# Kernel tuning notes

Hardware: AMD Instinct MI355X
Metric: run time of the kernel (lower is better)

The kernel has to match this reference:

```python
import jax, jax.numpy as jnp
import numpy as np

N = 50000          # nodes
E = 800000         # edges (avg degree 16)
NODE_IN, NODE_OUT = 64, 96
EDGE_IN, EDGE_OUT = 32, 32
CONV = [192, 192]  # hidden_conv_sizes
LIN = [192]        # hidden_linear_sizes
NUM_CLASSES = 2


def _linear_init(k, fan_in, fan_out):
    s = 1.0 / np.sqrt(fan_in)
    kw, kb = jax.random.split(k)
    W = jax.random.uniform(kw, (fan_in, fan_out), jnp.float32, -s, s)
    b = jax.random.uniform(kb, (fan_out,), jnp.float32, -s, s)
    return W, b


def setup_inputs() -> dict:
    key = jax.random.key(0)
    ks = jax.random.split(key, 10)
    node_feats = jax.random.normal(ks[0], (N, NODE_IN), jnp.float32)
    edge_feats = jax.random.normal(ks[1], (E, EDGE_IN), jnp.float32)
    src = jax.random.randint(ks[2], (E,), 0, N)
    dst = jax.random.randint(ks[3], (E,), 0, N)
    Wn, bn = _linear_init(ks[4], NODE_IN, NODE_OUT)
    We, be = _linear_init(ks[5], EDGE_IN, EDGE_OUT)
    Wc0, bc0 = _linear_init(ks[6], NODE_OUT + EDGE_OUT, CONV[0])
    Wc1, bc1 = _linear_init(ks[7], CONV[0], CONV[1])
    Wl0, bl0 = _linear_init(ks[8], CONV[1], LIN[0])
    Wo, bo = _linear_init(ks[9], LIN[0], NUM_CLASSES)
    return dict(node_feats=node_feats, edge_feats=edge_feats,
                Wn=Wn, bn=bn, We=We, be=be,
                Wc0=Wc0, bc0=bc0, Wc1=Wc1, bc1=bc1,
                Wl0=Wl0, bl0=bl0, Wo=Wo, bo=bo,
                src=src, dst=dst)


def reference(node_feats, edge_feats, Wn, bn, We, be, Wc0, bc0, Wc1, bc1,
              Wl0, bl0, Wo, bo, src, dst):
    ones = jnp.ones((E,), jnp.float32)
    deg_in = jnp.clip(jax.ops.segment_sum(ones, dst, num_segments=N), 1.0)
    deg_out = jnp.clip(jax.ops.segment_sum(ones, src, num_segments=N), 1.0)
    inv_in = jax.lax.rsqrt(deg_in)    # D_in^{-1/2}
    inv_out = jax.lax.rsqrt(deg_out)  # D_out^{-1/2}

    # EdgeLayer: per-edge linear, mean-aggregated onto destination nodes
    eh = edge_feats @ We + be                                   # [E, EDGE_OUT]
    edge_h = jax.nn.relu(
        jax.ops.segment_sum(eh, dst, num_segments=N) / deg_in[:, None])

    # NodeEmbeddingLayer: per-node linear
    node_h = jax.nn.relu(node_feats @ Wn + bn)                  # [N, NODE_OUT]

    h = jnp.concatenate([edge_h, node_h], axis=1)               # [N, EDGE_OUT+NODE_OUT]

    # dgl GraphConv (norm='both'): D_in^{-1/2} A D_out^{-1/2} h W + b
    # dropout is identity in eval mode
    for W, b in ((Wc0, bc0), (Wc1, bc1)):
        msg = (h * inv_out[:, None])[src]                       # [E, d] gather
        agg = jax.ops.segment_sum(msg, dst, num_segments=N) * inv_in[:, None]
        h = jax.nn.relu(agg @ W + b)

    h = jax.nn.relu(h @ Wl0 + bl0)
    return h @ Wo + bo                                          # [N, NUM_CLASSES]
```

## Files before the change

kernel.cpp:

```cpp
#include <hip/hip_runtime.h>

#define NN 50000
#define NE 800000
#define CAP 64

typedef unsigned short u16;
typedef __attribute__((ext_vector_type(8))) short bf8_t;
typedef __attribute__((ext_vector_type(4))) float f4_t;

__device__ __forceinline__ u16 f2b(float f) {
    unsigned u = __float_as_uint(f);
    unsigned r = u + 0x7FFF + ((u >> 16) & 1);
    return (u16)(r >> 16);
}

__global__ void build_k(const int* __restrict__ src, const int* __restrict__ dst,
                        int* __restrict__ cursor_in, int* __restrict__ deg_out,
                        int2* __restrict__ csr, int E) {
    int e = blockIdx.x * 256 + threadIdx.x;
    if (e < E) {
        int s = src[e];
        int d = dst[e];
        int p = atomicAdd(cursor_in + d, 1);
        csr[(d << 6) + p] = make_int2(s, e);
        atomicAdd(deg_out + s, 1);
    }
}

__global__ void make_inv_k(const int* __restrict__ deg_in, const int* __restrict__ deg_out,
                           float* __restrict__ inv_in, float* __restrict__ inv_out,
                           float* __restrict__ inv_mean, float* __restrict__ bcoef, int n) {
    int i = blockIdx.x * 256 + threadIdx.x;
    if (i < n) {
        int d_in = deg_in[i];
        float di = fmaxf((float)d_in, 1.0f);
        float dq = fmaxf((float)deg_out[i], 1.0f);
        inv_in[i]   = 1.0f / sqrtf(di);
        inv_out[i]  = 1.0f / sqrtf(dq);
        inv_mean[i] = 1.0f / di;
        bcoef[i]    = (d_in > 0) ? 1.0f : 0.0f;
    }
}

__global__ __launch_bounds__(256) void gather_e2_k(
    const float* __restrict__ ef, const int2* __restrict__ csr,
    const int* __restrict__ deg, float* __restrict__ efa) {
    const int lane = threadIdx.x & 63;
    const int node = __builtin_amdgcn_readfirstlane(blockIdx.x * 4 + (threadIdx.x >> 6));
    const int beg = node << 6;
    const int cnt = deg[node];
    const int off = lane & 31;
    const int half = lane >> 5;
    float acc = 0.0f;

    const int np = cnt >> 1;
    const int nb = np >> 3, rem = np & 7;
    int idx[8];
    if (nb > 0) {
#pragma unroll
        for (int j = 0; j < 8; ++j) idx[j] = csr[beg + 2 * j + half].y;
    }
    for (int b = 0; b < nb; ++b) {
        float lv[8];
#pragma unroll
        for (int j = 0; j < 8; ++j) lv[j] = ef[(size_t)idx[j] * 32 + off];
        int nidx[8];
        const int nbase = beg + 2 * (b + 1) * 8;
        if (b + 1 < nb) {
#pragma unroll
            for (int j = 0; j < 8; ++j) nidx[j] = csr[nbase + 2 * j + half].y;
        }
#pragma unroll
        for (int j = 0; j < 8; ++j) acc += lv[j];
        if (b + 1 < nb) {
#pragma unroll
            for (int j = 0; j < 8; ++j) idx[j] = nidx[j];
        }
    }
    const int tbase = beg + 2 * nb * 8;
    for (int t = 0; t < rem; ++t) acc += ef[(size_t)csr[tbase + 2 * t + half].y * 32 + off];
    if ((cnt & 1) && half == 0) acc += ef[(size_t)csr[beg + cnt - 1].y * 32 + off];

    acc += __shfl_down(acc, 32);
    if (lane < 32) efa[(size_t)node * 32 + off] = acc;
}

template <int D, int LPT>
__global__ __launch_bounds__(256) void gather_b2_k(
    const u16* __restrict__ h, const int2* __restrict__ csr,
    const int* __restrict__ deg, const float* __restrict__ inv_in,
    u16* __restrict__ agg) {
    constexpr int ACT = D / LPT;
    constexpr int NW = LPT / 2;
    const int lane = threadIdx.x & 63;
    const int node = __builtin_amdgcn_readfirstlane(blockIdx.x * 4 + (threadIdx.x >> 6));
    const int beg = node << 6;
    const int cnt = deg[node];
    const int off = (lane < ACT ? lane : ACT - 1) * LPT;

    float acc[LPT];
#pragma unroll
    for (int j = 0; j < LPT; ++j) acc[j] = 0.0f;

    const int nb = cnt >> 3, rem = cnt & 7;
    int idx[8];
    if (nb > 0) {
#pragma unroll
        for (int j = 0; j < 8; ++j) idx[j] = csr[beg + j].x;
    }
    for (int b = 0; b < nb; ++b) {
        unsigned lv[8][NW];
#pragma unroll
        for (int j = 0; j < 8; ++j) {
            const unsigned* p = (const unsigned*)(h + (size_t)idx[j] * D + off);
            if constexpr (NW == 2) {
                uint2 t = *(const uint2*)p;
                lv[j][0] = t.x; lv[j][1] = t.y;
            } else {
                lv[j][0] = *p;
            }
        }
        int nidx[8];
        const int nbase = beg + (b + 1) * 8;
        if (b + 1 < nb) {
#pragma unroll
            for (int j = 0; j < 8; ++j) nidx[j] = csr[nbase + j].x;
        }
#pragma unroll
        for (int j = 0; j < 8; ++j)
#pragma unroll
            for (int q = 0; q < NW; ++q) {
                unsigned u = lv[j][q];
                acc[2 * q]     += __uint_as_float(u << 16);
                acc[2 * q + 1] += __uint_as_float(u & 0xffff0000u);
            }
        if (b + 1 < nb) {
#pragma unroll
            for (int j = 0; j < 8; ++j) idx[j] = nidx[j];
        }
    }
    const int tbase = beg + nb * 8;
    for (int t = 0; t < rem; ++t) {
        const unsigned* p = (const unsigned*)(h + (size_t)csr[tbase + t].x * D + off);
#pragma unroll
        for (int q = 0; q < NW; ++q) {
            unsigned u = p[q];
            acc[2 * q]     += __uint_as_float(u << 16);
            acc[2 * q + 1] += __uint_as_float(u & 0xffff0000u);
        }
    }

    if (lane < ACT) {
        float sc = inv_in[node];
        unsigned o[NW];
#pragma unroll
        for (int q = 0; q < NW; ++q)
            o[q] = (unsigned)f2b(acc[2 * q] * sc) | ((unsigned)f2b(acc[2 * q + 1] * sc) << 16);
        unsigned* dp = (unsigned*)(agg + (size_t)node * D + off);
        if constexpr (NW == 2) {
            uint2 t; t.x = o[0]; t.y = o[1];
            *(uint2*)dp = t;
        } else {
            *dp = o[0];
        }
    }
}

template <int D_IN, int D_OUT, bool SCALE, bool BROW>
__global__ __launch_bounds__(256) void gemm_tile_k(
    const float* __restrict__ in, int in_stride,
    const float* __restrict__ W, const float* __restrict__ bias,
    const float* __restrict__ scale, const float* __restrict__ brow,
    const float* __restrict__ posts,
    u16* __restrict__ out, int out_stride, int n) {
    constexpr int TMW = 8;
    constexpr int ROWS = TMW * 4;
    constexpr int NOUT = (D_OUT + 63) / 64;
    __shared__ float s_in[ROWS * D_IN];

    const int tid = threadIdx.x;
    const int lane = tid & 63;
    const int wave = tid >> 6;
    const int row0 = blockIdx.x * ROWS;

    constexpr int NV = ROWS * D_IN / 4;
    for (int i = tid; i < NV; i += 256) {
        int m = i / (D_IN / 4);
        int kv = i % (D_IN / 4);
        int row = min(row0 + m, n - 1);
        float4 v = *(const float4*)(in + (size_t)row * in_stride + kv * 4);
        if (SCALE) {
            float s = scale[row];
            v.x *= s; v.y *= s; v.z *= s; v.w *= s;
        }
        *(float4*)(s_in + m * D_IN + kv * 4) = v;
    }
    __syncthreads();

    int f[NOUT], ff[NOUT];
    bool fok[NOUT];
    float bv[NOUT];
#pragma unroll
    for (int o = 0; o < NOUT; ++o) {
        f[o] = lane + 64 * o;
        fok[o] = (f[o] < D_OUT);
        ff[o] = fok[o] ? f[o] : 0;
        bv[o] = bias[ff[o]];
    }

    const float* s_my = s_in + wave * TMW * D_IN;

    float acc[NOUT][TMW];
#pragma unroll
    for (int o = 0; o < NOUT; ++o)
#pragma unroll
        for (int m = 0; m < TMW; ++m) acc[o][m] = 0.0f;

    for (int k = 0; k < D_IN; k += 4) {
        float w[4][NOUT];
#pragma unroll
        for (int j = 0; j < 4; ++j)
#pragma unroll
            for (int o = 0; o < NOUT; ++o) w[j][o] = W[(k + j) * D_OUT + ff[o]];
#pragma unroll
        for (int m = 0; m < TMW; ++m) {
            float4 a = *(const float4*)(s_my + m * D_IN + k);
#pragma unroll
            for (int o = 0; o < NOUT; ++o) {
                acc[o][m] = fmaf(a.x, w[0][o], acc[o][m]);
                acc[o][m] = fmaf(a.y, w[1][o], acc[o][m]);
                acc[o][m] = fmaf(a.z, w[2][o], acc[o][m]);
                acc[o][m] = fmaf(a.w, w[3][o], acc[o][m]);
            }
        }
    }

#pragma unroll
    for (int m = 0; m < TMW; ++m) {
        int row = row0 + wave * TMW + m;
        if (row < n) {
            float bc = BROW ? brow[row] : 1.0f;
            float pm = posts[row];
#pragma unroll
            for (int o = 0; o < NOUT; ++o) {
                if (!fok[o]) continue;
                float v = fmaxf(acc[o][m] + bv[o] * bc, 0.0f) * pm;
                out[(size_t)row * out_stride + f[o]] = f2b(v);
            }
        }
    }
}

template <int K>
__global__ void pack_w_k(const float* __restrict__ W, u16* __restrict__ Wp) {
    constexpr int KS = K / 32;
    int idx = blockIdx.x * 256 + threadIdx.x;
    if (idx >= 12 * KS * 64) return;
    int l = idx & 63;
    int s = (idx >> 6) % KS;
    int t = (idx >> 6) / KS;
    int col = t * 16 + (l & 15);
    int krow = s * 32 + ((l >> 4) * 8);
    u16 tmp[8] __attribute__((aligned(16)));
#pragma unroll
    for (int j = 0; j < 8; ++j) tmp[j] = f2b(W[(size_t)(krow + j) * 192 + col]);
    *(uint4*)(Wp + (size_t)idx * 8) = *(const uint4*)tmp;
}

template <int K>
__global__ __launch_bounds__(256) void mfma_gemm_k(
    const u16* __restrict__ A, const u16* __restrict__ Wp,
    const float* __restrict__ bias, const float* __restrict__ posts,
    u16* __restrict__ outB, int n) {
    constexpr int KS = K / 32;
    const int tid = threadIdx.x;
    const int lane = tid & 63;
    const int w = tid >> 6;
    const int row0 = blockIdx.x * 16;
    const int arow = row0 + (lane & 15);
    const int kbase = (lane >> 4) * 8;

    f4_t acc[3];
#pragma unroll
    for (int o = 0; o < 3; ++o) acc[o] = (f4_t){0.f, 0.f, 0.f, 0.f};

    const u16* ap = A + (size_t)arow * K + kbase;
#pragma unroll
    for (int s = 0; s < KS; ++s) {
        bf8_t af = *(const bf8_t*)(ap + s * 32);
#pragma unroll
        for (int o = 0; o < 3; ++o) {
            int t = w * 3 + o;
            bf8_t bf = *(const bf8_t*)(Wp + (size_t)((t * KS + s) * 64 + lane) * 8);
            acc[o] = __builtin_amdgcn_mfma_f32_16x16x32_bf16(af, bf, acc[o], 0, 0, 0);
        }
    }

    const int drow = row0 + (lane >> 4) * 4;
    const int dcol = lane & 15;
    float pm[4];
#pragma unroll
    for (int r = 0; r < 4; ++r) pm[r] = posts[drow + r];
#pragma unroll
    for (int o = 0; o < 3; ++o) {
        int col = (w * 3 + o) * 16 + dcol;
        float bv = bias[col];
#pragma unroll
        for (int r = 0; r < 4; ++r) {
            float v = fmaxf(acc[o][r] + bv, 0.0f) * pm[r];
            outB[(size_t)(drow + r) * 192 + col] = f2b(v);
        }
    }
}

__global__ __launch_bounds__(256) void mfma_fused_k(
    const u16* __restrict__ A,
    const u16* __restrict__ Wp1, const float* __restrict__ b1,
    const u16* __restrict__ Wp2, const float* __restrict__ b2,
    const float* __restrict__ Wo, const float* __restrict__ bo,
    float* __restrict__ out, int n) {
    constexpr int KS = 6;
    constexpr int S = 200;
    __shared__ float sbuf[16 * S];
    __shared__ float s_head[16][17][2];

    const int tid = threadIdx.x;
    const int lane = tid & 63;
    const int w = tid >> 6;
    const int row0 = blockIdx.x * 16;
    const int arow = row0 + (lane & 15);
    const int kbase = (lane >> 4) * 8;
    const int drow = (lane >> 4) * 4;
    const int dcol = lane & 15;

    f4_t acc[3];
#pragma unroll
    for (int o = 0; o < 3; ++o) acc[o] = (f4_t){0.f, 0.f, 0.f, 0.f};

    const u16* ap = A + (size_t)arow * 192 + kbase;
#pragma unroll
    for (int s = 0; s < KS; ++s) {
        bf8_t af = *(const bf8_t*)(ap + s * 32);
#pragma unroll
        for (int o = 0; o < 3; ++o) {
            int t = w * 3 + o;
            bf8_t bf = *(const bf8_t*)(Wp1 + (size_t)((t * KS + s) * 64 + lane) * 8);
            acc[o] = __builtin_amdgcn_mfma_f32_16x16x32_bf16(af, bf, acc[o], 0, 0, 0);
        }
    }

    u16* h2 = (u16*)sbuf;
#pragma unroll
    for (int o = 0; o < 3; ++o) {
        int col = (w * 3 + o) * 16 + dcol;
        float bv = b1[col];
#pragma unroll
        for (int r = 0; r < 4; ++r)
            h2[(drow + r) * S + col] = f2b(fmaxf(acc[o][r] + bv, 0.0f));
    }
    __syncthreads();

#pragma unroll
    for (int o = 0; o < 3; ++o) acc[o] = (f4_t){0.f, 0.f, 0.f, 0.f};
    const u16* hp = h2 + (lane & 15) * S + kbase;
#pragma unroll
    for (int s = 0; s < KS; ++s) {
        bf8_t af = *(const bf8_t*)(hp + s * 32);
#pragma unroll
        for (int o = 0; o < 3; ++o) {
            int t = w * 3 + o;
            bf8_t bf = *(const bf8_t*)(Wp2 + (size_t)((t * KS + s) * 64 + lane) * 8);
            acc[o] = __builtin_amdgcn_mfma_f32_16x16x32_bf16(af, bf, acc[o], 0, 0, 0);
        }
    }
    __syncthreads();

#pragma unroll
    for (int o = 0; o < 3; ++o) {
        int col = (w * 3 + o) * 16 + dcol;
        float bv = b2[col];
#pragma unroll
        for (int r = 0; r < 4; ++r)
            sbuf[(drow + r) * S + col] = fmaxf(acc[o][r] + bv, 0.0f);
    }
    __syncthreads();

    {
        int r = tid >> 4;
        int seg = tid & 15;
        const float* hr = sbuf + r * S + seg * 12;
        const float* wor = Wo + seg * 24;
        float p0 = 0.0f, p1 = 0.0f;
#pragma unroll
        for (int c = 0; c < 12; ++c) {
            float hv = hr[c];
            p0 = fmaf(hv, wor[c * 2 + 0], p0);
            p1 = fmaf(hv, wor[c * 2 + 1], p1);
        }
        s_head[r][seg][0] = p0;
        s_head[r][seg][1] = p1;
    }
    __syncthreads();
    if (tid < 32) {
        int r = tid >> 1, c = tid & 1;
        float sum = bo[c];
#pragma unroll
        for (int g = 0; g < 16; ++g) sum += s_head[r][g][c];
        int row = row0 + r;
        if (row < n) out[(size_t)row * 2 + c] = sum;
    }
}

extern "C" void kernel_launch(void* const* d_in, const int* in_sizes, int n_in,
                              void* d_out, int out_size, void* d_ws, size_t ws_size,
                              hipStream_t stream) {
    const float* node_feats = (const float*)d_in[0];
    const float* edge_feats = (const float*)d_in[1];
    const float* Wn  = (const float*)d_in[2];
    const float* bn  = (const float*)d_in[3];
    const float* We  = (const float*)d_in[4];
    const float* be  = (const float*)d_in[5];
    const float* Wc0 = (const float*)d_in[6];
    const float* bc0 = (const float*)d_in[7];
    const float* Wc1 = (const float*)d_in[8];
    const float* bc1 = (const float*)d_in[9];
    const float* Wl0 = (const float*)d_in[10];
    const float* bl0 = (const float*)d_in[11];
    const float* Wo  = (const float*)d_in[12];
    const float* bo  = (const float*)d_in[13];
    const int* src = (const int*)d_in[14];
    const int* dst = (const int*)d_in[15];
    float* out = (float*)d_out;

    const int N = NN, E = NE;

    int* din       = (int*)d_ws;
    int* dout      = din + N;
    int2* csr      = (int2*)(dout + N);
    float* inv_in   = (float*)(csr + (size_t)CAP * N);
    float* inv_out  = inv_in + N;
    float* inv_mean = inv_out + N;
    float* bcoef    = inv_mean + N;
    float* efa      = bcoef + N;
    u16* h0   = (u16*)(efa + (size_t)32 * N);
    u16* aggA = h0 + (size_t)128 * N;
    u16* h1   = aggA + (size_t)128 * N;
    u16* aggB = h1 + (size_t)192 * N;
    u16* Wp0  = aggB + (size_t)192 * N;
    u16* Wp1  = Wp0 + 128 * 192;
    u16* Wp2  = Wp1 + 192 * 192;

    hipMemsetAsync(d_ws, 0, (size_t)2 * N * sizeof(int), stream);

    const int GB32 = (N + 31) / 32;
    const int GB16 = N / 16;
    const int GW4  = (N + 3) / 4;

    pack_w_k<128><<<dim3(12), dim3(256), 0, stream>>>(Wc0, Wp0);
    pack_w_k<192><<<dim3(18), dim3(256), 0, stream>>>(Wc1, Wp1);
    pack_w_k<192><<<dim3(18), dim3(256), 0, stream>>>(Wl0, Wp2);

    build_k<<<dim3((E + 255) / 256), dim3(256), 0, stream>>>(src, dst, din, dout, csr, E);
    make_inv_k<<<dim3((N + 255) / 256), dim3(256), 0, stream>>>(din, dout, inv_in, inv_out,
                                                                inv_mean, bcoef, N);

    gather_e2_k<<<dim3(GW4), dim3(256), 0, stream>>>(edge_feats, csr, din, efa);
    gemm_tile_k<32, 32, true, true><<<dim3(GB32), dim3(256), 0, stream>>>(
        efa, 32, We, be, inv_mean, bcoef, inv_out, h0, 128, N);
    gemm_tile_k<64, 96, false, false><<<dim3(GB32), dim3(256), 0, stream>>>(
        node_feats, 64, Wn, bn, nullptr, nullptr, inv_out, h0 + 32, 128, N);

    gather_b2_k<128, 2><<<dim3(GW4), dim3(256), 0, stream>>>(h0, csr, din, inv_in, aggA);
    mfma_gemm_k<128><<<dim3(GB16), dim3(256), 0, stream>>>(aggA, Wp0, bc0, inv_out, h1, N);

    gather_b2_k<192, 4><<<dim3(GW4), dim3(256), 0, stream>>>(h1, csr, din, inv_in, aggB);
    mfma_fused_k<<<dim3(GB16), dim3(256), 0, stream>>>(aggB, Wp1, bc1, Wp2, bl0, Wo, bo,
                                                       out, N);
}
```

Before: 457.1 us.

## Split each node's neighbor gather across two waves with LDS reduction

Result: slower. 472.7 us (+3.4%).

```diff
diff --git a/kernel.cpp b/kernel.cpp
--- a/kernel.cpp
+++ b/kernel.cpp
@@ -42,58 +42,54 @@
     }
 }
 
-__global__ __launch_bounds__(256) void gather_e2_k(
+__global__ __launch_bounds__(256) void gather_e3_k(
     const float* __restrict__ ef, const int2* __restrict__ csr,
     const int* __restrict__ deg, float* __restrict__ efa) {
+    __shared__ float ep[2][32];
     const int lane = threadIdx.x & 63;
-    const int node = __builtin_amdgcn_readfirstlane(blockIdx.x * 4 + (threadIdx.x >> 6));
+    const int slot = threadIdx.x >> 7;
+    const int wh = (threadIdx.x >> 6) & 1;
+    const int node = __builtin_amdgcn_readfirstlane(blockIdx.x * 2 + slot);
     const int beg = node << 6;
     const int cnt = deg[node];
     const int off = lane & 31;
-    const int half = lane >> 5;
+    const int u = wh * 2 + (lane >> 5);
     float acc = 0.0f;
 
-    const int np = cnt >> 1;
-    const int nb = np >> 3, rem = np & 7;
-    int idx[8];
-    if (nb > 0) {
-#pragma unroll
-        for (int j = 0; j < 8; ++j) idx[j] = csr[beg + 2 * j + half].y;
-    }
-    for (int b = 0; b < nb; ++b) {
-        float lv[8];
-#pragma unroll
-        for (int j = 0; j < 8; ++j) lv[j] = ef[(size_t)idx[j] * 32 + off];
-        int nidx[8];
-        const int nbase = beg + 2 * (b + 1) * 8;
-        if (b + 1 < nb) {
-#pragma unroll
-            for (int j = 0; j < 8; ++j) nidx[j] = csr[nbase + 2 * j + half].y;
-        }
-#pragma unroll
-        for (int j = 0; j < 8; ++j) acc += lv[j];
-        if (b + 1 < nb) {
-#pragma unroll
-            for (int j = 0; j < 8; ++j) idx[j] = nidx[j];
-        }
-    }
-    const int tbase = beg + 2 * nb * 8;
-    for (int t = 0; t < rem; ++t) acc += ef[(size_t)csr[tbase + 2 * t + half].y * 32 + off];
-    if ((cnt & 1) && half == 0) acc += ef[(size_t)csr[beg + cnt - 1].y * 32 + off];
+    for (int base = u * 4; base + 4 <= cnt; base += 16) {
+        int idx[4];
+#pragma unroll
+        for (int j = 0; j < 4; ++j) idx[j] = csr[beg + base + j].y;
+        float lv[4];
+#pragma unroll
+        for (int j = 0; j < 4; ++j) lv[j] = ef[(size_t)idx[j] * 32 + off];
+#pragma unroll
+        for (int j = 0; j < 4; ++j) acc += lv[j];
+    }
+    {
+        const int tb = cnt & ~3, tc = cnt & 3;
+        if (tc && ((tb >> 2) & 3) == u)
+            for (int t = 0; t < tc; ++t) acc += ef[(size_t)csr[beg + tb + t].y * 32 + off];
+    }
 
     acc += __shfl_down(acc, 32);
-    if (lane < 32) efa[(size_t)node * 32 + off] = acc;
+    if (wh == 0 && lane < 32) ep[slot][lane] = acc;
+    __syncthreads();
+    if (wh == 1 && lane < 32) efa[(size_t)node * 32 + lane] = acc + ep[slot][lane];
 }
 
 template <int D, int LPT>
-__global__ __launch_bounds__(256) void gather_b2_k(
+__global__ __launch_bounds__(256) void gather_b3_k(
     const u16* __restrict__ h, const int2* __restrict__ csr,
     const int* __restrict__ deg, const float* __restrict__ inv_in,
     u16* __restrict__ agg) {
     constexpr int ACT = D / LPT;
     constexpr int NW = LPT / 2;
+    __shared__ float part[2][D];
     const int lane = threadIdx.x & 63;
-    const int node = __builtin_amdgcn_readfirstlane(blockIdx.x * 4 + (threadIdx.x >> 6));
+    const int slot = threadIdx.x >> 7;
+    const int wh = (threadIdx.x >> 6) & 1;
+    const int node = __builtin_amdgcn_readfirstlane(blockIdx.x * 2 + slot);
     const int beg = node << 6;
     const int cnt = deg[node];
     const int off = (lane < ACT ? lane : ACT - 1) * LPT;
@@ -102,13 +98,10 @@
 #pragma unroll
     for (int j = 0; j < LPT; ++j) acc[j] = 0.0f;
 
-    const int nb = cnt >> 3, rem = cnt & 7;
-    int idx[8];
-    if (nb > 0) {
-#pragma unroll
-        for (int j = 0; j < 8; ++j) idx[j] = csr[beg + j].x;
-    }
-    for (int b = 0; b < nb; ++b) {
+    for (int base = wh * 8; base + 8 <= cnt; base += 16) {
+        int idx[8];
+#pragma unroll
+        for (int j = 0; j < 8; ++j) idx[j] = csr[beg + base + j].x;
         unsigned lv[8][NW];
 #pragma unroll
         for (int j = 0; j < 8; ++j) {
@@ -120,12 +113,6 @@
                 lv[j][0] = *p;
             }
         }
-        int nidx[8];
-        const int nbase = beg + (b + 1) * 8;
-        if (b + 1 < nb) {
-#pragma unroll
-            for (int j = 0; j < 8; ++j) nidx[j] = csr[nbase + j].x;
-        }
 #pragma unroll
         for (int j = 0; j < 8; ++j)
 #pragma unroll
@@ -134,28 +121,36 @@
                 acc[2 * q]     += __uint_as_float(u << 16);
                 acc[2 * q + 1] += __uint_as_float(u & 0xffff0000u);
             }
-        if (b + 1 < nb) {
-#pragma unroll
-            for (int j = 0; j < 8; ++j) idx[j] = nidx[j];
-        }
-    }
-    const int tbase = beg + nb * 8;
-    for (int t = 0; t < rem; ++t) {
-        const unsigned* p = (const unsigned*)(h + (size_t)csr[tbase + t].x * D + off);
-#pragma unroll
-        for (int q = 0; q < NW; ++q) {
-            unsigned u = p[q];
-            acc[2 * q]     += __uint_as_float(u << 16);
-            acc[2 * q + 1] += __uint_as_float(u & 0xffff0000u);
-        }
-    }
-
-    if (lane < ACT) {
+    }
+    {
+        const int tb = cnt & ~7, tc = cnt & 7;
+        if (tc && ((tb >> 3) & 1) == wh) {
+            for (int t = 0; t < tc; ++t) {
+                const unsigned* p = (const unsigned*)(h + (size_t)csr[beg + tb + t].x * D + off);
+#pragma unroll
+                for (int q = 0; q < NW; ++q) {
+                    unsigned u = p[q];
+                    acc[2 * q]     += __uint_as_float(u << 16);
+                    acc[2 * q + 1] += __uint_as_float(u & 0xffff0000u);
+                }
+            }
+        }
+    }
+
+    if (wh == 0 && lane < ACT) {
+#pragma unroll
+        for (int j = 0; j < LPT; ++j) part[slot][lane * LPT + j] = acc[j];
+    }
+    __syncthreads();
+    if (wh == 1 && lane < ACT) {
         float sc = inv_in[node];
         unsigned o[NW];
 #pragma unroll
-        for (int q = 0; q < NW; ++q)
-            o[q] = (unsigned)f2b(acc[2 * q] * sc) | ((unsigned)f2b(acc[2 * q + 1] * sc) << 16);
+        for (int q = 0; q < NW; ++q) {
+            float v0 = (acc[2 * q]     + part[slot][lane * LPT + 2 * q])     * sc;
+            float v1 = (acc[2 * q + 1] + part[slot][lane * LPT + 2 * q + 1]) * sc;
+            o[q] = (unsigned)f2b(v0) | ((unsigned)f2b(v1) << 16);
+        }
         unsigned* dp = (unsigned*)(agg + (size_t)node * D + off);
         if constexpr (NW == 2) {
             uint2 t; t.x = o[0]; t.y = o[1];
@@ -454,7 +449,7 @@
 
     const int GB32 = (N + 31) / 32;
     const int GB16 = N / 16;
-    const int GW4  = (N + 3) / 4;
+    const int GN2  = N / 2;
 
     pack_w_k<128><<<dim3(12), dim3(256), 0, stream>>>(Wc0, Wp0);
     pack_w_k<192><<<dim3(18), dim3(256), 0, stream>>>(Wc1, Wp1);
@@ -464,16 +459,16 @@
     make_inv_k<<<dim3((N + 255) / 256), dim3(256), 0, stream>>>(din, dout, inv_in, inv_out,
                                                                 inv_mean, bcoef, N);
 
-    gather_e2_k<<<dim3(GW4), dim3(256), 0, stream>>>(edge_feats, csr, din, efa);
+    gather_e3_k<<<dim3(GN2), dim3(256), 0, stream>>>(edge_feats, csr, din, efa);
     gemm_tile_k<32, 32, true, true><<<dim3(GB32), dim3(256), 0, stream>>>(
         efa, 32, We, be, inv_mean, bcoef, inv_out, h0, 128, N);
     gemm_tile_k<64, 96, false, false><<<dim3(GB32), dim3(256), 0, stream>>>(
         node_feats, 64, Wn, bn, nullptr, nullptr, inv_out, h0 + 32, 128, N);
 
-    gather_b2_k<128, 2><<<dim3(GW4), dim3(256), 0, stream>>>(h0, csr, din, inv_in, aggA);
+    gather_b3_k<128, 2><<<dim3(GN2), dim3(256), 0, stream>>>(h0, csr, din, inv_in, aggA);
     mfma_gemm_k<128><<<dim3(GB16), dim3(256), 0, stream>>>(aggA, Wp0, bc0, inv_out, h1, N);
 
-    gather_b2_k<192, 4><<<dim3(GW4), dim3(256), 0, stream>>>(h1, csr, din, inv_in, aggB);
+    gather_b3_k<192, 4><<<dim3(GN2), dim3(256), 0, stream>>>(h1, csr, din, inv_in, aggB);
     mfma_fused_k<<<dim3(GB16), dim3(256), 0, stream>>>(aggB, Wp1, bc1, Wp2, bl0, Wo, bo,
                                                        out, N);
 }
```
